# Kernel optimization log

Measured on AMD Instinct MI355X. Metric: run time of the kernel, lower is better.

The kernel has to match this reference:

```python
import jax, jax.numpy as jnp
import numpy as np

N_NODES = 100000
N_EDGES = 3200000

def setup_inputs() -> dict:
    key = jax.random.key(0)
    ks = jax.random.split(key, 6)
    x = jax.random.normal(ks[0], (N_NODES, 40), dtype=jnp.float32)
    src = jax.random.randint(ks[1], (N_EDGES,), 0, N_NODES, dtype=jnp.int32)
    dst = jax.random.randint(ks[2], (N_EDGES,), 0, N_NODES, dtype=jnp.int32)
    W1 = jax.random.normal(ks[3], (10, 128), dtype=jnp.float32) * 0.1
    b1 = jnp.zeros((128,), dtype=jnp.float32)
    W2 = jax.random.normal(ks[4], (128, 64), dtype=jnp.float32) * 0.1
    b2 = jnp.zeros((64,), dtype=jnp.float32)
    return {"x": x, "src": src, "dst": dst, "W1": W1, "b1": b1, "W2": W2, "b2": b2}


def reference(x, src, dst, W1, b1, W2, b2):
    N = x.shape[0]
    xs = x[:, 15:25]  # forward slices features to in_dim=10
    ones = jnp.ones(src.shape[0], dtype=x.dtype)
    deg_out = jax.ops.segment_sum(ones, src, num_segments=N)  # out-degree of src nodes
    deg_in = jax.ops.segment_sum(ones, dst, num_segments=N)   # in-degree of dst nodes
    # DGL GraphConv norm='both': clamp zero degrees to 1, symmetric 1/sqrt norm
    norm_s = jnp.where(deg_out > 0, deg_out, 1.0) ** -0.5
    norm_d = jnp.where(deg_in > 0, deg_in, 1.0) ** -0.5
    # aggregate-then-transform (in_dim < hidden_dim path in DGL)
    msgs = (xs * norm_s[:, None])[src]                         # [E, 10]
    agg = jax.ops.segment_sum(msgs, dst, num_segments=N)      # [N, 10]
    agg = agg * norm_d[:, None]
    h = agg @ W1 + b1                                          # GraphConv weight + bias
    return h @ W2 + b2                                         # linear head
```

## Files before the change

kernel.cpp:

```cpp
#include <hip/hip_runtime.h>
#include <hip/hip_fp16.h>


#define NF    10
#define COLS  40
#define OFF   15
#define H1    128
#define H2    64

#define BSH   7
#define BW    128
#define NBIN  782
#define NBINP 784
#define GS    16
#define RND   16u
#define CAPH  6400
#define PRCAP 4864
#define SENT  0xFFFFFFFFu
#define NBLKB 320
#define CHUNK 10000
#define BT    512

#define DBLK    128
#define DCHUNKS 32
#define DRANGES 4
#define DRNG    25000
#define DRNG4   6250
#define DEDGE   100000

typedef unsigned int u32;
typedef unsigned short u16;
typedef unsigned char u8;

__device__ __forceinline__ float2 h2f(u32 u) {
    __half2 h;
    *reinterpret_cast<u32*>(&h) = u;
    return __half22float2(h);
}
__device__ __forceinline__ u32 f2h(float a, float b) {
    __half2 h = __float22half2_rn(make_float2(a, b));
    return *reinterpret_cast<u32*>(&h);
}

__global__ void __launch_bounds__(BT, 4)
fusedA_kernel(const int* __restrict__ src, const int* __restrict__ dst,
              const float* __restrict__ W1, const float* __restrict__ b1,
              const float* __restrict__ W2, const float* __restrict__ b2,
              float* __restrict__ Wc, float* __restrict__ bc,
              u32* __restrict__ gcur, u32* __restrict__ partial32,
              u32* __restrict__ srt, int E, int N) {
    __shared__ union {
        struct { u32 hist[NBINP], lofs[NBINP], gbase[NBINP], lcur[NBINP];
                 u32 stage[CHUNK]; u8 sbin[CHUNK]; } pb;
        struct { u32 cnt[DRNG4]; } dg;
    } sh;
    int blk = blockIdx.x;
    int t = threadIdx.x;

    if (blk < DBLK) {
        int c = blk & (DCHUNKS - 1);
        int r = blk >> 5;
        u32* cnt = sh.dg.cnt;
        for (int i = t; i < DRNG4; i += BT) cnt[i] = 0;
        __syncthreads();
        int base = r * DRNG;
        int e0 = c * DEDGE, e1 = min(E, e0 + DEDGE);
        int nv4 = (e1 - e0) >> 2;
        const int4* s4 = (const int4*)(src + e0);
        for (int i = t; i < nv4; i += BT) {
            int4 s = s4[i];
            int a0 = s.x - base, a1 = s.y - base, a2 = s.z - base, a3 = s.w - base;
            if ((u32)a0 < (u32)DRNG) atomicAdd(&cnt[a0 >> 2], 1u << ((a0 & 3) << 3));
            if ((u32)a1 < (u32)DRNG) atomicAdd(&cnt[a1 >> 2], 1u << ((a1 & 3) << 3));
            if ((u32)a2 < (u32)DRNG) atomicAdd(&cnt[a2 >> 2], 1u << ((a2 & 3) << 3));
            if ((u32)a3 < (u32)DRNG) atomicAdd(&cnt[a3 >> 2], 1u << ((a3 & 3) << 3));
        }
        __syncthreads();
        u32* d32 = partial32 + ((size_t)c * N + base) / 4;
        for (int i = t; i < DRNG4; i += BT) d32[i] = cnt[i];
    } else if (blk < DBLK + NBLKB) {
        u32* hist = sh.pb.hist;
        u32* lofs = sh.pb.lofs;
        u32* gbase = sh.pb.gbase;
        u32* lcur = sh.pb.lcur;
        u32* stage = sh.pb.stage;
        u8*  sbin = sh.pb.sbin;
        for (int i = t; i < NBINP; i += BT) hist[i] = 0;
        __syncthreads();

        int e0 = (blk - DBLK) * CHUNK;
        int m = min(E - e0, CHUNK);
        int m4 = m >> 2;
        const int4* d4 = (const int4*)(dst + e0);
        const int4* s4 = (const int4*)(src + e0);

        for (int i4 = t; i4 < m4; i4 += BT) {
            int4 d = d4[i4];
            atomicAdd(&hist[d.x >> BSH], 1u);
            atomicAdd(&hist[d.y >> BSH], 1u);
            atomicAdd(&hist[d.z >> BSH], 1u);
            atomicAdd(&hist[d.w >> BSH], 1u);
        }
        for (int e = e0 + 4 * m4 + t; e < e0 + m; e += BT)
            atomicAdd(&hist[dst[e] >> BSH], 1u);
        __syncthreads();

        if (t < 64) {
            u32 c[13];
            u32 seg = 0;
#pragma unroll
            for (int q = 0; q < 13; ++q) {
                int idx = t * 13 + q;
                c[q] = (idx < NBINP) ? hist[idx] : 0u;
                seg += c[q];
            }
            u32 x = seg;
#pragma unroll
            for (int off = 1; off < 64; off <<= 1) {
                u32 v = (u32)__shfl_up((int)x, off, 64);
                if (t >= off) x += v;
            }
            u32 run = x - seg;
#pragma unroll
            for (int q = 0; q < 13; ++q) {
                int idx = t * 13 + q;
                if (idx < NBINP) lofs[idx] = run;
                run += c[q];
            }
        }
        __syncthreads();

        for (int b = t; b < NBIN; b += BT) {
            u32 h = hist[b];
            u32 r = (h + (RND - 1u)) & ~(RND - 1u);
            gbase[b] = r ? atomicAdd(&gcur[b * GS], r) : 0u;
            lcur[b] = lofs[b];
        }
        __syncthreads();

        for (int i4 = t; i4 < m4; i4 += BT) {
            int4 d = d4[i4];
            int4 s = s4[i4];
#define SC1(d_, s_) { int b_ = (d_) >> BSH; u32 p_ = atomicAdd(&lcur[b_], 1u); \
        stage[p_] = ((u32)(s_) << BSH) | (u32)((d_) & (BW - 1)); sbin[p_] = (u8)b_; }
            SC1(d.x, s.x); SC1(d.y, s.y); SC1(d.z, s.z); SC1(d.w, s.w);
        }
        for (int e = e0 + 4 * m4 + t; e < e0 + m; e += BT) {
            int d_ = dst[e], s_ = src[e];
            SC1(d_, s_);
        }
#undef SC1
        __syncthreads();

        {
            u32 th1 = lofs[256], th2 = lofs[512], th3 = lofs[768];
            for (int i = t; i < m; i += BT) {
                u32 ui = (u32)i;
                u32 k = (u32)(ui >= th1) + (u32)(ui >= th2) + (u32)(ui >= th3);
                u32 b = (k << 8) + sbin[i];
                u32 idx = gbase[b] + ui - lofs[b];
                if (idx < CAPH) srt[(size_t)b * CAPH + idx] = stage[i];
            }
        }
        for (int b = t; b < NBIN; b += BT) {
            u32 h = hist[b];
            if (!h) continue;
            u32 r = (h + (RND - 1u)) & ~(RND - 1u);
            for (u32 k = h; k < r; ++k) {
                u32 idx = gbase[b] + k;
                if (idx < CAPH) srt[(size_t)b * CAPH + idx] = SENT;
            }
        }
    } else {
        for (int i = t; i < NF * H2; i += BT) {
            int k = i >> 6, j = i & 63;
            float acc = 0.f;
            for (int mm = 0; mm < H1; ++mm) acc += W1[k * H1 + mm] * W2[mm * H2 + j];
            Wc[i] = acc;
        }
        for (int j = t; j < H2; j += BT) {
            float a = b2[j];
            for (int mm = 0; mm < H1; ++mm) a += b1[mm] * W2[mm * H2 + j];
            bc[j] = a;
        }
    }
}

__global__ void __launch_bounds__(256)
xsn_kernel(const float* __restrict__ x, const u8* __restrict__ partial,
           u16* __restrict__ xsn, int N) {
    int n = blockIdx.x * blockDim.x + threadIdx.x;
    if (n >= N) return;
    u32 d = 0;
#pragma unroll 4
    for (int c = 0; c < DCHUNKS; ++c) d += partial[(size_t)c * N + n];
    float norm = rsqrtf(d > 0 ? (float)d : 1.f);
    const float* xr = x + (size_t)n * COLS + OFF;
    float v[NF];
#pragma unroll
    for (int k = 0; k < NF; ++k) v[k] = xr[k] * norm;
    uint4* xo = (uint4*)(xsn + ((size_t)n << 4));
    uint4 w0, w1;
    w0.x = f2h(v[0], v[1]); w0.y = f2h(v[2], v[3]);
    w0.z = f2h(v[4], v[5]); w0.w = f2h(v[6], v[7]);
    w1.x = f2h(v[8], v[9]); w1.y = 0u; w1.z = 0u; w1.w = 0u;
    xo[0] = w0;
    xo[1] = w1;
}

__global__ void __launch_bounds__(256, 6)
passC_kernel(const u32* __restrict__ srt, const u32* __restrict__ gcur,
             const u16* __restrict__ xsn, const float* __restrict__ Wc,
             const float* __restrict__ bc, float* __restrict__ out, int N) {
    __shared__ u32 sorted[PRCAP];
    __shared__ u32 cnt[BW];
    __shared__ u32 cur[BW];
    __shared__ float sW[NF * H2];
    __shared__ float sb[H2];
    int t = threadIdx.x;
    for (int i = t; i < NF * H2; i += 256) sW[i] = Wc[i];
    if (t < H2) sb[t] = bc[t];
    if (t < BW) cnt[t] = 0;
    __syncthreads();

    int b = blockIdx.x;
    const u32* reg = srt + (size_t)b * CAPH;
    u32 m = gcur[b * GS];
    if (m > CAPH) m = CAPH;

    for (u32 e = t; e < m; e += 256) {
        u32 v = reg[e];
        if (v != SENT) atomicAdd(&cnt[v & (BW - 1)], 1u);
    }
    __syncthreads();

    if (t < 64) {
        u32 c0 = cnt[t * 2], c1 = cnt[t * 2 + 1];
        u32 seg = c0 + c1;
        u32 x = seg;
#pragma unroll
        for (int off = 1; off < 64; off <<= 1) {
            u32 v = (u32)__shfl_up((int)x, off, 64);
            if (t >= off) x += v;
        }
        u32 run = x - seg;
        cur[t * 2] = run; run += c0;
        cur[t * 2 + 1] = run;
    }
    __syncthreads();

    for (u32 e = t; e < m; e += 256) {
        u32 v = reg[e];
        if (v == SENT) continue;
        u32 p = atomicAdd(&cur[v & (BW - 1)], 1u);
        if (p < PRCAP) sorted[p] = v >> BSH;
    }
    __syncthreads();

    int node_local = t >> 2;
    int j = t & 3;
    int jb = j << 4;
#pragma unroll
    for (int sub = 0; sub < 2; ++sub) {
        int node = sub * 64 + node_local;
        u32 c   = cnt[node];
        u32 end = cur[node];
        if (end > PRCAP) end = PRCAP;
        u32 st  = (end >= c) ? end - c : 0u;
        float r0=0.f,r1=0.f,r2=0.f,r3=0.f,r4=0.f,r5=0.f,r6=0.f,r7=0.f,r8=0.f,r9=0.f;
#pragma unroll 2
        for (u32 e = st + j; e < end; e += 4) {
            const u32* xr = (const u32*)(xsn + ((size_t)sorted[e] << 4));
            uint4 p0 = *(const uint4*)xr;
            u32 p1 = xr[4];
            float2 f;
            f = h2f(p0.x); r0 += f.x; r1 += f.y;
            f = h2f(p0.y); r2 += f.x; r3 += f.y;
            f = h2f(p0.z); r4 += f.x; r5 += f.y;
            f = h2f(p0.w); r6 += f.x; r7 += f.y;
            f = h2f(p1);   r8 += f.x; r9 += f.y;
        }
#define QRED(r) r += __shfl_xor(r, 1, 64); r += __shfl_xor(r, 2, 64)
        QRED(r0); QRED(r1); QRED(r2); QRED(r3); QRED(r4);
        QRED(r5); QRED(r6); QRED(r7); QRED(r8); QRED(r9);
#undef QRED
        int n = (b << BSH) + node;
        if (n < N) {
            float norm = rsqrtf(c > 0 ? (float)c : 1.f);
            r0 *= norm; r1 *= norm; r2 *= norm; r3 *= norm; r4 *= norm;
            r5 *= norm; r6 *= norm; r7 *= norm; r8 *= norm; r9 *= norm;
            float o[16];
#pragma unroll
            for (int q = 0; q < 16; ++q) o[q] = sb[jb + q];
            float rr[NF] = {r0,r1,r2,r3,r4,r5,r6,r7,r8,r9};
#pragma unroll
            for (int k = 0; k < NF; ++k) {
                float a = rr[k];
#pragma unroll
                for (int q = 0; q < 16; ++q) o[q] += a * sW[k * H2 + jb + q];
            }
            float* op = out + (size_t)n * H2 + jb;
            *(float4*)(op)      = make_float4(o[0], o[1], o[2], o[3]);
            *(float4*)(op + 4)  = make_float4(o[4], o[5], o[6], o[7]);
            *(float4*)(op + 8)  = make_float4(o[8], o[9], o[10], o[11]);
            *(float4*)(op + 12) = make_float4(o[12], o[13], o[14], o[15]);
        }
    }
}

extern "C" void kernel_launch(void* const* d_in, const int* in_sizes, int n_in,
                              void* d_out, int out_size, void* d_ws, size_t ws_size,
                              hipStream_t stream) {
    const float* x   = (const float*)d_in[0];
    const int*   src = (const int*)d_in[1];
    const int*   dst = (const int*)d_in[2];
    const float* W1  = (const float*)d_in[3];
    const float* b1  = (const float*)d_in[4];
    const float* W2  = (const float*)d_in[5];
    const float* b2  = (const float*)d_in[6];
    float* out = (float*)d_out;

    const int N = in_sizes[0] / COLS;
    const int E = in_sizes[1];

    float* ws = (float*)d_ws;
    float* Wc   = ws;
    float* bc   = Wc + NF * H2;
    u32*   gcur = (u32*)(bc + H2);
    size_t off_u32 = (size_t)(NF * H2 + H2) + (size_t)NBIN * GS;
    off_u32 = (off_u32 + 15) & ~(size_t)15;
    u16*   xsn = (u16*)((u32*)d_ws + off_u32);
    u32*   srt = (u32*)d_ws + off_u32 + (size_t)N * 8;
    u32*   partial32 = srt + (size_t)NBIN * CAPH;
    const u8* partial8 = (const u8*)partial32;

    hipMemsetAsync(gcur, 0, (size_t)NBIN * GS * sizeof(u32), stream);

    fusedA_kernel<<<DBLK + NBLKB + 1, BT, 0, stream>>>(
        src, dst, W1, b1, W2, b2, Wc, bc, gcur, partial32, srt, E, N);

    xsn_kernel<<<(N + 255) / 256, 256, 0, stream>>>(x, partial8, xsn, N);

    passC_kernel<<<NBIN, 256, 0, stream>>>(srt, gcur, xsn, Wc, bc, out, N);
}
```

Measured before the change: 179.5 us.

## Widen passC to 512 threads with register-cached bin entries and per-group counters

The per-bin gather kernel now runs 512 threads per block instead of 256, so each thread handles one node slot rather than looping over two. Bin entries are loaded once into a 13-entry register array and reused for both the counting and the scatter passes, removing the second global read. Shared atomics are split across four per-wavegroup counter arrays to reduce contention, which adds an extra combine step and another barrier. The fixed KMAX bound assumes at most 6656 entries per bin (CAPH is 6400), and the wider block with more registers could lower occupancy.

```diff
diff --git a/kernel.cpp b/kernel.cpp
--- a/kernel.cpp
+++ b/kernel.cpp
@@ -20,6 +20,9 @@
 #define NBLKB 320
 #define CHUNK 10000
 #define BT    512
+
+#define PCT   512
+#define KMAX  13
 
 #define DBLK    128
 #define DCHUNKS 32
@@ -208,103 +211,118 @@
     xo[1] = w1;
 }
 
-__global__ void __launch_bounds__(256, 6)
+__global__ void __launch_bounds__(PCT, 6)
 passC_kernel(const u32* __restrict__ srt, const u32* __restrict__ gcur,
              const u16* __restrict__ xsn, const float* __restrict__ Wc,
              const float* __restrict__ bc, float* __restrict__ out, int N) {
     __shared__ u32 sorted[PRCAP];
-    __shared__ u32 cnt[BW];
-    __shared__ u32 cur[BW];
+    __shared__ u32 cnt4[4][BW];
+    __shared__ u32 cur4[4][BW];
+    __shared__ u32 tot[BW];
+    __shared__ u32 sbase[BW];
     __shared__ float sW[NF * H2];
     __shared__ float sb[H2];
     int t = threadIdx.x;
-    for (int i = t; i < NF * H2; i += 256) sW[i] = Wc[i];
+    for (int i = t; i < NF * H2; i += PCT) sW[i] = Wc[i];
     if (t < H2) sb[t] = bc[t];
-    if (t < BW) cnt[t] = 0;
+    ((u32*)cnt4)[t] = 0;
     __syncthreads();
 
     int b = blockIdx.x;
     const u32* reg = srt + (size_t)b * CAPH;
     u32 m = gcur[b * GS];
     if (m > CAPH) m = CAPH;
-
-    for (u32 e = t; e < m; e += 256) {
-        u32 v = reg[e];
-        if (v != SENT) atomicAdd(&cnt[v & (BW - 1)], 1u);
-    }
-    __syncthreads();
-
+    int g = t >> 7;
+
+    u32 v[KMAX];
+#pragma unroll
+    for (int k = 0; k < KMAX; ++k) {
+        u32 e = (u32)t + (u32)(k * PCT);
+        v[k] = (e < m) ? reg[e] : SENT;
+        if (v[k] != SENT) atomicAdd(&cnt4[g][v[k] & (BW - 1)], 1u);
+    }
+    __syncthreads();
+
+    if (t < BW) tot[t] = cnt4[0][t] + cnt4[1][t] + cnt4[2][t] + cnt4[3][t];
+    __syncthreads();
     if (t < 64) {
-        u32 c0 = cnt[t * 2], c1 = cnt[t * 2 + 1];
+        u32 c0 = tot[t * 2], c1 = tot[t * 2 + 1];
         u32 seg = c0 + c1;
         u32 x = seg;
 #pragma unroll
         for (int off = 1; off < 64; off <<= 1) {
-            u32 v = (u32)__shfl_up((int)x, off, 64);
-            if (t >= off) x += v;
+            u32 w = (u32)__shfl_up((int)x, off, 64);
+            if (t >= off) x += w;
         }
         u32 run = x - seg;
-        cur[t * 2] = run; run += c0;
-        cur[t * 2 + 1] = run;
-    }
-    __syncthreads();
-
-    for (u32 e = t; e < m; e += 256) {
-        u32 v = reg[e];
-        if (v == SENT) continue;
-        u32 p = atomicAdd(&cur[v & (BW - 1)], 1u);
-        if (p < PRCAP) sorted[p] = v >> BSH;
-    }
-    __syncthreads();
-
-    int node_local = t >> 2;
+        sbase[t * 2] = run;
+        sbase[t * 2 + 1] = run + c0;
+    }
+    __syncthreads();
+    {
+        int n = t & (BW - 1);
+        int gg = t >> 7;
+        u32 o = sbase[n];
+        if (gg > 0) o += cnt4[0][n];
+        if (gg > 1) o += cnt4[1][n];
+        if (gg > 2) o += cnt4[2][n];
+        cur4[gg][n] = o;
+    }
+    __syncthreads();
+
+#pragma unroll
+    for (int k = 0; k < KMAX; ++k) {
+        if (v[k] != SENT) {
+            u32 p = atomicAdd(&cur4[g][v[k] & (BW - 1)], 1u);
+            if (p < PRCAP) sorted[p] = v[k] >> BSH;
+        }
+    }
+    __syncthreads();
+
+    int node = t >> 2;
     int j = t & 3;
     int jb = j << 4;
-#pragma unroll
-    for (int sub = 0; sub < 2; ++sub) {
-        int node = sub * 64 + node_local;
-        u32 c   = cnt[node];
-        u32 end = cur[node];
-        if (end > PRCAP) end = PRCAP;
-        u32 st  = (end >= c) ? end - c : 0u;
-        float r0=0.f,r1=0.f,r2=0.f,r3=0.f,r4=0.f,r5=0.f,r6=0.f,r7=0.f,r8=0.f,r9=0.f;
+    u32 c   = tot[node];
+    u32 st  = sbase[node];
+    u32 end = st + c;
+    if (end > PRCAP) end = PRCAP;
+    float r0=0.f,r1=0.f,r2=0.f,r3=0.f,r4=0.f,r5=0.f,r6=0.f,r7=0.f,r8=0.f,r9=0.f;
 #pragma unroll 2
-        for (u32 e = st + j; e < end; e += 4) {
-            const u32* xr = (const u32*)(xsn + ((size_t)sorted[e] << 4));
-            uint4 p0 = *(const uint4*)xr;
-            u32 p1 = xr[4];
-            float2 f;
-            f = h2f(p0.x); r0 += f.x; r1 += f.y;
-            f = h2f(p0.y); r2 += f.x; r3 += f.y;
-            f = h2f(p0.z); r4 += f.x; r5 += f.y;
-            f = h2f(p0.w); r6 += f.x; r7 += f.y;
-            f = h2f(p1);   r8 += f.x; r9 += f.y;
-        }
+    for (u32 e = st + j; e < end; e += 4) {
+        const u32* xr = (const u32*)(xsn + ((size_t)sorted[e] << 4));
+        uint4 p0 = *(const uint4*)xr;
+        u32 p1 = xr[4];
+        float2 f;
+        f = h2f(p0.x); r0 += f.x; r1 += f.y;
+        f = h2f(p0.y); r2 += f.x; r3 += f.y;
+        f = h2f(p0.z); r4 += f.x; r5 += f.y;
+        f = h2f(p0.w); r6 += f.x; r7 += f.y;
+        f = h2f(p1);   r8 += f.x; r9 += f.y;
+    }
 #define QRED(r) r += __shfl_xor(r, 1, 64); r += __shfl_xor(r, 2, 64)
-        QRED(r0); QRED(r1); QRED(r2); QRED(r3); QRED(r4);
-        QRED(r5); QRED(r6); QRED(r7); QRED(r8); QRED(r9);
+    QRED(r0); QRED(r1); QRED(r2); QRED(r3); QRED(r4);
+    QRED(r5); QRED(r6); QRED(r7); QRED(r8); QRED(r9);
 #undef QRED
-        int n = (b << BSH) + node;
-        if (n < N) {
-            float norm = rsqrtf(c > 0 ? (float)c : 1.f);
-            r0 *= norm; r1 *= norm; r2 *= norm; r3 *= norm; r4 *= norm;
-            r5 *= norm; r6 *= norm; r7 *= norm; r8 *= norm; r9 *= norm;
-            float o[16];
-#pragma unroll
-            for (int q = 0; q < 16; ++q) o[q] = sb[jb + q];
-            float rr[NF] = {r0,r1,r2,r3,r4,r5,r6,r7,r8,r9};
-#pragma unroll
-            for (int k = 0; k < NF; ++k) {
-                float a = rr[k];
-#pragma unroll
-                for (int q = 0; q < 16; ++q) o[q] += a * sW[k * H2 + jb + q];
-            }
-            float* op = out + (size_t)n * H2 + jb;
-            *(float4*)(op)      = make_float4(o[0], o[1], o[2], o[3]);
-            *(float4*)(op + 4)  = make_float4(o[4], o[5], o[6], o[7]);
-            *(float4*)(op + 8)  = make_float4(o[8], o[9], o[10], o[11]);
-            *(float4*)(op + 12) = make_float4(o[12], o[13], o[14], o[15]);
-        }
+    int n = (b << BSH) + node;
+    if (n < N) {
+        float norm = rsqrtf(c > 0 ? (float)c : 1.f);
+        r0 *= norm; r1 *= norm; r2 *= norm; r3 *= norm; r4 *= norm;
+        r5 *= norm; r6 *= norm; r7 *= norm; r8 *= norm; r9 *= norm;
+        float o[16];
+#pragma unroll
+        for (int q = 0; q < 16; ++q) o[q] = sb[jb + q];
+        float rr[NF] = {r0,r1,r2,r3,r4,r5,r6,r7,r8,r9};
+#pragma unroll
+        for (int k = 0; k < NF; ++k) {
+            float a = rr[k];
+#pragma unroll
+            for (int q = 0; q < 16; ++q) o[q] += a * sW[k * H2 + jb + q];
+        }
+        float* op = out + (size_t)n * H2 + jb;
+        *(float4*)(op)      = make_float4(o[0], o[1], o[2], o[3]);
+        *(float4*)(op + 4)  = make_float4(o[4], o[5], o[6], o[7]);
+        *(float4*)(op + 8)  = make_float4(o[8], o[9], o[10], o[11]);
+        *(float4*)(op + 12) = make_float4(o[12], o[13], o[14], o[15]);
     }
 }
 
@@ -341,5 +359,5 @@
 
     xsn_kernel<<<(N + 255) / 256, 256, 0, stream>>>(x, partial8, xsn, N);
 
-    passC_kernel<<<NBIN, 256, 0, stream>>>(srt, gcur, xsn, Wc, bc, out, N);
-}
+    passC_kernel<<<NBIN, PCT, 0, stream>>>(srt, gcur, xsn, Wc, bc, out, N);
+}
```

Result: no change. 177.4 us (-1.1%).
